# Kernel optimization log

Hardware: AMD Instinct MI355X
Metric: run time of the kernel (lower is better)

Reference implementation:

```python
import jax, jax.numpy as jnp
import numpy as np

D = 16        # d_model
DFF = 128     # ffn hidden
H_NN = 128    # pairwise-MLP hidden
RES = 1.0     # res_ratio (undefined global in source; standard residual)
EPS = 1e-6


def setup_inputs() -> dict:
    key = jax.random.key(0)
    ks = jax.random.split(key, 16)
    B, G, L = 8, 1, 256
    def n(k, shape, s=0.05):
        return jax.random.normal(k, shape, jnp.float32) * s
    return dict(
        x=jax.random.normal(ks[0], (B, G, L, D), jnp.float32),
        mask=jnp.zeros((B, G, L, L), jnp.float32),
        wq=n(ks[1], (D, D)), bq=jnp.zeros((D,), jnp.float32),
        wk=n(ks[2], (D, D)), bk=jnp.zeros((D,), jnp.float32),
        wv=n(ks[3], (D, D)), bv=jnp.zeros((D,), jnp.float32),
        wo=n(ks[4], (D, D)), bo=jnp.zeros((D,), jnp.float32),
        nn_w1=n(ks[5], (2 * D, H_NN)), nn_b1=jnp.zeros((H_NN,), jnp.float32),
        nn_w2=n(ks[6], (H_NN, 1)), nn_b2=jnp.zeros((1,), jnp.float32),
        f1=n(ks[7], (D, DFF)), f1b=jnp.zeros((DFF,), jnp.float32),
        f2=n(ks[8], (DFF, D)), f2b=jnp.zeros((D,), jnp.float32),
        g1=jnp.ones((D,), jnp.float32), be1=jnp.zeros((D,), jnp.float32),
        g2=jnp.ones((D,), jnp.float32), be2=jnp.zeros((D,), jnp.float32),
    )


def _layernorm(x, g, b):
    m = jnp.mean(x, -1, keepdims=True)
    v = jnp.var(x, -1, keepdims=True)
    return (x - m) * jax.lax.rsqrt(v + EPS) * g + b


def reference(x, mask, wq, bq, wk, bk, wv, bv, wo, bo,
              nn_w1, nn_b1, nn_w2, nn_b2,
              f1, f1b, f2, f2b, g1, be1, g2, be2):
    # projections: (B,G,L,D)
    q = x @ wq + bq
    k = x @ wk + bk
    v = x @ wv + bv
    # pairwise relation-network attention.
    # NN(concat([q_i, k_j])) first layer splits as q_i @ W1[:D] + k_j @ W1[D:]
    w1q, w1k = nn_w1[:D], nn_w1[D:]
    w2 = nn_w2[:, 0]
    qa = q @ w1q  # (B,G,L,H)
    kb = k @ w1k
    h1 = jax.nn.relu(qa[:, :, :, None, :] + kb[:, :, None, :, :] + nn_b1)  # (B,G,Lq,Lk,H)
    logits = jnp.einsum('bgijh,h->bgij', h1, w2) + nn_b2[0]
    # make_sym: NN(concat([k_j, q_i])) -> k_j @ W1[:D] + q_i @ W1[D:]
    ka = k @ w1q
    qb = q @ w1k
    h2 = jax.nn.relu(qb[:, :, :, None, :] + ka[:, :, None, :, :] + nn_b1)
    logits = logits + jnp.einsum('bgijh,h->bgij', h2, w2) + nn_b2[0]
    logits = logits + mask * -1e9
    attn = jax.nn.softmax(logits, axis=-1)          # (B,G,Lq,Lk)
    ctx = jnp.einsum('bgij,bgjd->bgid', attn, v)    # (B,G,L,D)
    attn_out = ctx @ wo + bo
    out1 = _layernorm(RES * x + (2.0 - RES) * attn_out, g1, be1)
    ffn = jax.nn.relu(out1 @ f1 + f1b) @ f2 + f2b
    out2 = _layernorm(RES * out1 + (2.0 - RES) * ffn, g2, be2)
    return out2
```

## Files before the change

kernel.cpp:

```cpp
#include <hip/hip_runtime.h>
#include <hip/hip_bf16.h>

typedef __hip_bfloat16 bf16;

constexpr int DIM  = 16;
constexpr int HNN  = 128;
constexpr int SEQ  = 256;
constexpr int BAT  = 8;
constexpr int ROWS = BAT * SEQ;

__device__ __forceinline__ bool is_f32(const void* g1) {
  return ((const unsigned*)g1)[0] == 0x3F800000u;
}
__device__ __forceinline__ float ld(const void* p, long i, bool f32) {
  return f32 ? ((const float*)p)[i]
             : __bfloat162float(((const bf16*)p)[i]);
}

__global__ __launch_bounds__(128) void prep_kernel(
    const void* __restrict__ x,
    const void* __restrict__ wq, const void* __restrict__ bq,
    const void* __restrict__ wk, const void* __restrict__ bk,
    const void* __restrict__ wv, const void* __restrict__ bv,
    const void* __restrict__ nn_w1, const void* __restrict__ nn_b1,
    const void* __restrict__ g1flag,
    float* __restrict__ qa, float* __restrict__ qb,
    float* __restrict__ kbT, float* __restrict__ kaT,
    float* __restrict__ vT)
{
  const bool f32 = is_f32(g1flag);
  const int row = blockIdx.x;
  const int tid = threadIdx.x;
  __shared__ float xs[DIM], qs[DIM], ks[DIM], vs[DIM];

  if (tid < DIM) xs[tid] = ld(x, (long)row * DIM + tid, f32);
  __syncthreads();

  if (tid < 3 * DIM) {
    const int which = tid >> 4, d = tid & 15;
    const void* w  = (which == 0) ? wq : (which == 1) ? wk : wv;
    const void* bb = (which == 0) ? bq : (which == 1) ? bk : bv;
    float acc = ld(bb, d, f32);
    #pragma unroll
    for (int e = 0; e < DIM; e++) acc += xs[e] * ld(w, e * DIM + d, f32);
    if (which == 0) qs[d] = acc;
    else if (which == 1) ks[d] = acc;
    else vs[d] = acc;
  }
  __syncthreads();

  float qw1q = 0.f, qw1k = 0.f, kw1q = 0.f, kw1k = 0.f;
  #pragma unroll
  for (int d = 0; d < DIM; d++) {
    float a = ld(nn_w1, d * HNN + tid, f32);
    float b = ld(nn_w1, (DIM + d) * HNN + tid, f32);
    qw1q += qs[d] * a;  qw1k += qs[d] * b;
    kw1q += ks[d] * a;  kw1k += ks[d] * b;
  }
  const float b1 = ld(nn_b1, tid, f32);
  qa[row * HNN + tid]   = qw1q;
  qb[row * HNN + tid]   = qw1k;
  kbT[tid * ROWS + row] = kw1k + b1;
  kaT[tid * ROWS + row] = kw1q + b1;
  if (tid < DIM) vT[tid * ROWS + row] = vs[tid];
}

__global__ __launch_bounds__(256) void attn_kernel(
    const void* __restrict__ x,  const void* __restrict__ mask,
    const void* __restrict__ wo, const void* __restrict__ bo,
    const void* __restrict__ nn_w2, const void* __restrict__ nn_b2,
    const void* __restrict__ f1, const void* __restrict__ f1b,
    const void* __restrict__ f2, const void* __restrict__ f2b,
    const void* __restrict__ g1, const void* __restrict__ be1,
    const void* __restrict__ g2, const void* __restrict__ be2,
    const float* __restrict__ qa, const float* __restrict__ qb,
    const float* __restrict__ kbT, const float* __restrict__ kaT,
    const float* __restrict__ vT,
    void* __restrict__ out)
{
  const bool f32 = is_f32(g1);
  const int blk = blockIdx.x;
  const int bi  = blk >> 8;
  const int j   = threadIdx.x;

  __shared__ float sqa[HNN], sqb[HNN], sw2[HNN];
  __shared__ float red[SEQ], pbuf[SEQ];
  __shared__ float part[DIM][17];
  __shared__ float ctxs[DIM], r1[DIM], o1[DIM], hid[HNN], r2[DIM];

  if (j < HNN) {
    sqa[j] = qa[(size_t)blk * HNN + j];
    sqb[j] = qb[(size_t)blk * HNN + j];
    sw2[j] = ld(nn_w2, j, f32);
  }
  __syncthreads();

  const int col = bi * SEQ + j;
  float acc = 0.f;
  #pragma unroll 4
  for (int h = 0; h < HNN; h++) {
    float kb = kbT[h * ROWS + col];
    float ka = kaT[h * ROWS + col];
    acc += sw2[h] * (fmaxf(sqa[h] + kb, 0.f) + fmaxf(sqb[h] + ka, 0.f));
  }
  float logit = acc + 2.f * ld(nn_b2, 0, f32)
              + ld(mask, (long)blk * SEQ + j, f32) * -1e9f;

  red[j] = logit;
  __syncthreads();
  for (int s = 128; s > 0; s >>= 1) {
    if (j < s) red[j] = fmaxf(red[j], red[j + s]);
    __syncthreads();
  }
  const float mx = red[0];
  __syncthreads();
  const float e = __expf(logit - mx);
  pbuf[j] = e;
  red[j]  = e;
  __syncthreads();
  for (int s = 128; s > 0; s >>= 1) {
    if (j < s) red[j] += red[j + s];
    __syncthreads();
  }
  const float inv = 1.f / red[0];

  {
    const int d = j & 15, c = j >> 4;
    float p = 0.f;
    #pragma unroll
    for (int jj = 0; jj < 16; jj++)
      p += pbuf[c * 16 + jj] * vT[d * ROWS + bi * SEQ + c * 16 + jj];
    part[d][c] = p;
  }
  __syncthreads();
  if (j < DIM) {
    float s = 0.f;
    #pragma unroll
    for (int c = 0; c < 16; c++) s += part[j][c];
    ctxs[j] = s * inv;
  }
  __syncthreads();

  if (j < DIM) {
    float ao = ld(bo, j, f32);
    #pragma unroll
    for (int d = 0; d < DIM; d++) ao += ctxs[d] * ld(wo, d * DIM + j, f32);
    r1[j] = ld(x, (long)blk * DIM + j, f32) + ao;
  }
  __syncthreads();

  if (j < DIM) {
    float m = 0.f;
    #pragma unroll
    for (int d = 0; d < DIM; d++) m += r1[d];
    m *= (1.f / DIM);
    float v = 0.f;
    #pragma unroll
    for (int d = 0; d < DIM; d++) { float t = r1[d] - m; v += t * t; }
    v *= (1.f / DIM);
    o1[j] = (r1[j] - m) * rsqrtf(v + 1e-6f) * ld(g1, j, f32) + ld(be1, j, f32);
  }
  __syncthreads();

  if (j < HNN) {
    float a = ld(f1b, j, f32);
    #pragma unroll
    for (int d = 0; d < DIM; d++) a += o1[d] * ld(f1, d * HNN + j, f32);
    hid[j] = fmaxf(a, 0.f);
  }
  __syncthreads();

  if (j < DIM) {
    float a = ld(f2b, j, f32);
    for (int h = 0; h < HNN; h++) a += hid[h] * ld(f2, h * DIM + j, f32);
    r2[j] = o1[j] + a;
  }
  __syncthreads();

  if (j < DIM) {
    float m = 0.f;
    #pragma unroll
    for (int d = 0; d < DIM; d++) m += r2[d];
    m *= (1.f / DIM);
    float v = 0.f;
    #pragma unroll
    for (int d = 0; d < DIM; d++) { float t = r2[d] - m; v += t * t; }
    v *= (1.f / DIM);
    float val = (r2[j] - m) * rsqrtf(v + 1e-6f) * ld(g2, j, f32) + ld(be2, j, f32);
    if (f32) ((float*)out)[(long)blk * DIM + j] = val;
    else     ((bf16*)out)[(long)blk * DIM + j] = __float2bfloat16(val);
  }
}

extern "C" void kernel_launch(void* const* d_in, const int* in_sizes, int n_in,
                              void* d_out, int out_size, void* d_ws, size_t ws_size,
                              hipStream_t stream) {
  const void* x     = d_in[0];
  const void* mask  = d_in[1];
  const void* wq    = d_in[2];
  const void* bq    = d_in[3];
  const void* wk    = d_in[4];
  const void* bk    = d_in[5];
  const void* wv    = d_in[6];
  const void* bv    = d_in[7];
  const void* wo    = d_in[8];
  const void* bo    = d_in[9];
  const void* nn_w1 = d_in[10];
  const void* nn_b1 = d_in[11];
  const void* nn_w2 = d_in[12];
  const void* nn_b2 = d_in[13];
  const void* f1    = d_in[14];
  const void* f1b   = d_in[15];
  const void* f2    = d_in[16];
  const void* f2b   = d_in[17];
  const void* g1    = d_in[18];
  const void* be1   = d_in[19];
  const void* g2    = d_in[20];
  const void* be2   = d_in[21];

  float* qa  = (float*)d_ws;
  float* qb  = qa  + (size_t)ROWS * HNN;
  float* kbT = qb  + (size_t)ROWS * HNN;
  float* kaT = kbT + (size_t)ROWS * HNN;
  float* vT  = kaT + (size_t)ROWS * HNN;

  prep_kernel<<<ROWS, 128, 0, stream>>>(x, wq, bq, wk, bk, wv, bv, nn_w1, nn_b1,
                                        g1, qa, qb, kbT, kaT, vT);
  attn_kernel<<<ROWS, 256, 0, stream>>>(x, mask, wo, bo, nn_w2, nn_b2,
                                        f1, f1b, f2, f2b, g1, be1, g2, be2,
                                        qa, qb, kbT, kaT, vT, d_out);
}
```

Measured before the change: 147.1 us.

## Process four query rows per block and interleave key tensors for float4 loads

The attention kernel now handles four query rows per block instead of one. Each loaded key feature (ka/kb, interleaved into a single float2-packed buffer so one float4 load fetches two hidden units) is reused across four queries, cutting global key traffic by roughly four. Block reductions are replaced by wavefront shuffles, V is staged in shared memory, and w2 is converted once in the prep kernel. The cost is more registers and shared memory per block and a quarter as many blocks, which lowers parallelism.

Result: faster. 138.0 us (-6.2%).

```diff
diff --git a/kernel.cpp b/kernel.cpp
--- a/kernel.cpp
+++ b/kernel.cpp
@@ -8,6 +8,8 @@
 constexpr int SEQ  = 256;
 constexpr int BAT  = 8;
 constexpr int ROWS = BAT * SEQ;
+constexpr int QT   = 4;
+constexpr int NBLK = ROWS / QT;
 
 __device__ __forceinline__ bool is_f32(const void* g1) {
   return ((const unsigned*)g1)[0] == 0x3F800000u;
@@ -23,10 +25,9 @@
     const void* __restrict__ wk, const void* __restrict__ bk,
     const void* __restrict__ wv, const void* __restrict__ bv,
     const void* __restrict__ nn_w1, const void* __restrict__ nn_b1,
-    const void* __restrict__ g1flag,
+    const void* __restrict__ nn_w2, const void* __restrict__ g1flag,
     float* __restrict__ qa, float* __restrict__ qb,
-    float* __restrict__ kbT, float* __restrict__ kaT,
-    float* __restrict__ vT)
+    float* __restrict__ kkT, float* __restrict__ vT, float* __restrict__ w2f)
 {
   const bool f32 = is_f32(g1flag);
   const int row = blockIdx.x;
@@ -58,137 +59,163 @@
     kw1q += ks[d] * a;  kw1k += ks[d] * b;
   }
   const float b1 = ld(nn_b1, tid, f32);
-  qa[row * HNN + tid]   = qw1q;
-  qb[row * HNN + tid]   = qw1k;
-  kbT[tid * ROWS + row] = kw1k + b1;
-  kaT[tid * ROWS + row] = kw1q + b1;
+  qa[row * HNN + tid] = qw1q;
+  qb[row * HNN + tid] = qw1k;
+  ((float2*)kkT)[((size_t)(tid >> 1) * ROWS + row) * 2 + (tid & 1)] =
+      make_float2(kw1k + b1, kw1q + b1);
   if (tid < DIM) vT[tid * ROWS + row] = vs[tid];
+  if (row == 0) w2f[tid] = ld(nn_w2, tid, f32);
 }
 
 __global__ __launch_bounds__(256) void attn_kernel(
     const void* __restrict__ x,  const void* __restrict__ mask,
     const void* __restrict__ wo, const void* __restrict__ bo,
-    const void* __restrict__ nn_w2, const void* __restrict__ nn_b2,
+    const void* __restrict__ nn_b2,
     const void* __restrict__ f1, const void* __restrict__ f1b,
     const void* __restrict__ f2, const void* __restrict__ f2b,
     const void* __restrict__ g1, const void* __restrict__ be1,
     const void* __restrict__ g2, const void* __restrict__ be2,
     const float* __restrict__ qa, const float* __restrict__ qb,
-    const float* __restrict__ kbT, const float* __restrict__ kaT,
-    const float* __restrict__ vT,
+    const float* __restrict__ kkT, const float* __restrict__ vT,
+    const float* __restrict__ w2f,
     void* __restrict__ out)
 {
   const bool f32 = is_f32(g1);
-  const int blk = blockIdx.x;
-  const int bi  = blk >> 8;
-  const int j   = threadIdx.x;
-
-  __shared__ float sqa[HNN], sqb[HNN], sw2[HNN];
-  __shared__ float red[SEQ], pbuf[SEQ];
-  __shared__ float part[DIM][17];
-  __shared__ float ctxs[DIM], r1[DIM], o1[DIM], hid[HNN], r2[DIM];
-
-  if (j < HNN) {
-    sqa[j] = qa[(size_t)blk * HNN + j];
-    sqb[j] = qb[(size_t)blk * HNN + j];
-    sw2[j] = ld(nn_w2, j, f32);
-  }
-  __syncthreads();
-
-  const int col = bi * SEQ + j;
-  float acc = 0.f;
-  #pragma unroll 4
-  for (int h = 0; h < HNN; h++) {
-    float kb = kbT[h * ROWS + col];
-    float ka = kaT[h * ROWS + col];
-    acc += sw2[h] * (fmaxf(sqa[h] + kb, 0.f) + fmaxf(sqb[h] + ka, 0.f));
-  }
-  float logit = acc + 2.f * ld(nn_b2, 0, f32)
-              + ld(mask, (long)blk * SEQ + j, f32) * -1e9f;
-
-  red[j] = logit;
-  __syncthreads();
-  for (int s = 128; s > 0; s >>= 1) {
-    if (j < s) red[j] = fmaxf(red[j], red[j + s]);
-    __syncthreads();
-  }
-  const float mx = red[0];
-  __syncthreads();
-  const float e = __expf(logit - mx);
-  pbuf[j] = e;
-  red[j]  = e;
-  __syncthreads();
-  for (int s = 128; s > 0; s >>= 1) {
-    if (j < s) red[j] += red[j + s];
-    __syncthreads();
-  }
-  const float inv = 1.f / red[0];
-
-  {
-    const int d = j & 15, c = j >> 4;
-    float p = 0.f;
-    #pragma unroll
-    for (int jj = 0; jj < 16; jj++)
-      p += pbuf[c * 16 + jj] * vT[d * ROWS + bi * SEQ + c * 16 + jj];
-    part[d][c] = p;
-  }
-  __syncthreads();
-  if (j < DIM) {
+  const int blk  = blockIdx.x;
+  const int bi   = blk >> 6;
+  const int i0   = (blk & 63) * QT;
+  const int t    = threadIdx.x;
+  const int j    = t;
+  const int col  = bi * SEQ + j;
+  const int lane = t & 63, wv = t >> 6;
+
+  __shared__ float pb[QT][SEQ];
+  __shared__ float vbufT[SEQ][DIM + 1];
+  __shared__ float wred[2][QT][4];
+  __shared__ float ctxs[QT][DIM];
+  __shared__ float tmpA[QT][DIM];
+  __shared__ float tmpB[QT][DIM];
+  __shared__ float hids[QT][HNN];
+
+  #pragma unroll
+  for (int d = 0; d < DIM; ++d) vbufT[j][d] = vT[d * ROWS + col];
+
+  const float* qaB = qa + (size_t)(bi * SEQ + i0) * HNN;
+  const float* qbB = qb + (size_t)(bi * SEQ + i0) * HNN;
+  float acc[QT] = {0.f, 0.f, 0.f, 0.f};
+  #pragma unroll 2
+  for (int hp = 0; hp < HNN / 2; ++hp) {
+    const float4 kk = ((const float4*)kkT)[(size_t)hp * ROWS + col];
+    const float w0 = w2f[2 * hp], w1 = w2f[2 * hp + 1];
+    #pragma unroll
+    for (int ii = 0; ii < QT; ++ii) {
+      const float* qai = qaB + ii * HNN;
+      const float* qbi = qbB + ii * HNN;
+      float s0 = fmaxf(qai[2 * hp]     + kk.x, 0.f) + fmaxf(qbi[2 * hp]     + kk.y, 0.f);
+      float s1 = fmaxf(qai[2 * hp + 1] + kk.z, 0.f) + fmaxf(qbi[2 * hp + 1] + kk.w, 0.f);
+      acc[ii] = fmaf(w0, s0, acc[ii]);
+      acc[ii] = fmaf(w1, s1, acc[ii]);
+    }
+  }
+
+  const float b2v = ld(nn_b2, 0, f32);
+  float la[QT], e[QT];
+  #pragma unroll
+  for (int ii = 0; ii < QT; ++ii)
+    la[ii] = acc[ii] + 2.f * b2v
+           + ld(mask, ((size_t)bi * SEQ + (i0 + ii)) * SEQ + j, f32) * -1e9f;
+
+  #pragma unroll
+  for (int ii = 0; ii < QT; ++ii) {
+    float m = la[ii];
+    #pragma unroll
+    for (int off = 32; off > 0; off >>= 1) m = fmaxf(m, __shfl_xor(m, off, 64));
+    if (lane == 0) wred[0][ii][wv] = m;
+  }
+  __syncthreads();
+  #pragma unroll
+  for (int ii = 0; ii < QT; ++ii) {
+    const float mx = fmaxf(fmaxf(wred[0][ii][0], wred[0][ii][1]),
+                           fmaxf(wred[0][ii][2], wred[0][ii][3]));
+    const float ev = __expf(la[ii] - mx);
+    e[ii] = ev;
+    float s = ev;
+    #pragma unroll
+    for (int off = 32; off > 0; off >>= 1) s += __shfl_xor(s, off, 64);
+    if (lane == 0) wred[1][ii][wv] = s;
+    pb[ii][j] = ev;
+  }
+  __syncthreads();
+
+  if (t < QT * DIM) {
+    const int ii = t >> 4, d = t & 15;
     float s = 0.f;
-    #pragma unroll
-    for (int c = 0; c < 16; c++) s += part[j][c];
-    ctxs[j] = s * inv;
-  }
-  __syncthreads();
-
-  if (j < DIM) {
-    float ao = ld(bo, j, f32);
-    #pragma unroll
-    for (int d = 0; d < DIM; d++) ao += ctxs[d] * ld(wo, d * DIM + j, f32);
-    r1[j] = ld(x, (long)blk * DIM + j, f32) + ao;
-  }
-  __syncthreads();
-
-  if (j < DIM) {
+    #pragma unroll 8
+    for (int jj = 0; jj < SEQ; ++jj) s += pb[ii][jj] * vbufT[jj][d];
+    const float inv = 1.f / (wred[1][ii][0] + wred[1][ii][1] +
+                             wred[1][ii][2] + wred[1][ii][3]);
+    ctxs[ii][d] = s * inv;
+  }
+  __syncthreads();
+
+  if (t < QT * DIM) {
+    const int ii = t >> 4, d = t & 15;
+    float ao = ld(bo, d, f32);
+    #pragma unroll
+    for (int dd = 0; dd < DIM; ++dd) ao += ctxs[ii][dd] * ld(wo, dd * DIM + d, f32);
+    tmpA[ii][d] = ld(x, ((size_t)(bi * SEQ + i0 + ii)) * DIM + d, f32) + ao;
+  }
+  __syncthreads();
+
+  if (t < QT * DIM) {
+    const int ii = t >> 4, d = t & 15;
     float m = 0.f;
     #pragma unroll
-    for (int d = 0; d < DIM; d++) m += r1[d];
+    for (int dd = 0; dd < DIM; ++dd) m += tmpA[ii][dd];
     m *= (1.f / DIM);
     float v = 0.f;
     #pragma unroll
-    for (int d = 0; d < DIM; d++) { float t = r1[d] - m; v += t * t; }
+    for (int dd = 0; dd < DIM; ++dd) { float z = tmpA[ii][dd] - m; v += z * z; }
     v *= (1.f / DIM);
-    o1[j] = (r1[j] - m) * rsqrtf(v + 1e-6f) * ld(g1, j, f32) + ld(be1, j, f32);
-  }
-  __syncthreads();
-
-  if (j < HNN) {
-    float a = ld(f1b, j, f32);
-    #pragma unroll
-    for (int d = 0; d < DIM; d++) a += o1[d] * ld(f1, d * HNN + j, f32);
-    hid[j] = fmaxf(a, 0.f);
-  }
-  __syncthreads();
-
-  if (j < DIM) {
-    float a = ld(f2b, j, f32);
-    for (int h = 0; h < HNN; h++) a += hid[h] * ld(f2, h * DIM + j, f32);
-    r2[j] = o1[j] + a;
-  }
-  __syncthreads();
-
-  if (j < DIM) {
+    tmpB[ii][d] = (tmpA[ii][d] - m) * rsqrtf(v + 1e-6f) * ld(g1, d, f32)
+                + ld(be1, d, f32);
+  }
+  __syncthreads();
+
+  #pragma unroll
+  for (int p = 0; p < 2; ++p) {
+    const int ii = (t >> 7) + 2 * p;
+    const int h  = t & 127;
+    float a = ld(f1b, h, f32);
+    #pragma unroll
+    for (int dd = 0; dd < DIM; ++dd) a += tmpB[ii][dd] * ld(f1, dd * HNN + h, f32);
+    hids[ii][h] = fmaxf(a, 0.f);
+  }
+  __syncthreads();
+
+  if (t < QT * DIM) {
+    const int ii = t >> 4, d = t & 15;
+    float a = ld(f2b, d, f32);
+    for (int h = 0; h < HNN; ++h) a += hids[ii][h] * ld(f2, h * DIM + d, f32);
+    tmpA[ii][d] = tmpB[ii][d] + a;
+  }
+  __syncthreads();
+
+  if (t < QT * DIM) {
+    const int ii = t >> 4, d = t & 15;
     float m = 0.f;
     #pragma unroll
-    for (int d = 0; d < DIM; d++) m += r2[d];
+    for (int dd = 0; dd < DIM; ++dd) m += tmpA[ii][dd];
     m *= (1.f / DIM);
     float v = 0.f;
     #pragma unroll
-    for (int d = 0; d < DIM; d++) { float t = r2[d] - m; v += t * t; }
+    for (int dd = 0; dd < DIM; ++dd) { float z = tmpA[ii][dd] - m; v += z * z; }
     v *= (1.f / DIM);
-    float val = (r2[j] - m) * rsqrtf(v + 1e-6f) * ld(g2, j, f32) + ld(be2, j, f32);
-    if (f32) ((float*)out)[(long)blk * DIM + j] = val;
-    else     ((bf16*)out)[(long)blk * DIM + j] = __float2bfloat16(val);
+    const float val = (tmpA[ii][d] - m) * rsqrtf(v + 1e-6f) * ld(g2, d, f32)
+                    + ld(be2, d, f32);
+    const long oidx = ((long)(bi * SEQ + i0 + ii)) * DIM + d;
+    if (f32) ((float*)out)[oidx] = val;
+    else     ((bf16*)out)[oidx] = __float2bfloat16(val);
   }
 }
 
@@ -220,13 +247,13 @@
 
   float* qa  = (float*)d_ws;
   float* qb  = qa  + (size_t)ROWS * HNN;
-  float* kbT = qb  + (size_t)ROWS * HNN;
-  float* kaT = kbT + (size_t)ROWS * HNN;
-  float* vT  = kaT + (size_t)ROWS * HNN;
+  float* kkT = qb  + (size_t)ROWS * HNN;
+  float* vT  = kkT + (size_t)ROWS * HNN * 2;
+  float* w2f = vT  + (size_t)DIM * ROWS;
 
   prep_kernel<<<ROWS, 128, 0, stream>>>(x, wq, bq, wk, bk, wv, bv, nn_w1, nn_b1,
-                                        g1, qa, qb, kbT, kaT, vT);
-  attn_kernel<<<ROWS, 256, 0, stream>>>(x, mask, wo, bo, nn_w2, nn_b2,
+                                        nn_w2, g1, qa, qb, kkT, vT, w2f);
+  attn_kernel<<<NBLK, 256, 0, stream>>>(x, mask, wo, bo, nn_b2,
                                         f1, f1b, f2, f2b, g1, be1, g2, be2,
-                                        qa, qb, kbT, kaT, vT, d_out);
-}
+                                        qa, qb, kkT, vT, w2f, d_out);
+}
```

## Split pairwise logits into query-tiled kernel with split-H partials and shuffle softmax

Applied to the files above, without the earlier changes.

Moves the pairwise relation-MLP logit computation into its own kernel. Each block handles 4 queries and one quarter of the hidden dimension, so every loaded key feature is reused across 4 queries, and float4-interleaved ka/kb layouts vectorize the loads. Partial logits are written to a workspace and summed in a tail kernel. The tail kernel uses wave shuffles for the softmax reductions, stages V in shared memory and parallelizes the FFN second layer. This adds a third launch and an extra global round-trip of 4×ROWS×SEQ partial logits in exchange for less redundant key traffic and more parallelism.

Result: faster. 127.1 us (-13.6%).

```diff
diff --git a/kernel.cpp b/kernel.cpp
--- a/kernel.cpp
+++ b/kernel.cpp
@@ -8,6 +8,10 @@
 constexpr int SEQ  = 256;
 constexpr int BAT  = 8;
 constexpr int ROWS = BAT * SEQ;
+constexpr int HP   = HNN / 2;
+constexpr int QT   = 4;
+constexpr int NQT  = ROWS / QT;
+constexpr int QHP  = 16;
 
 __device__ __forceinline__ bool is_f32(const void* g1) {
   return ((const unsigned*)g1)[0] == 0x3F800000u;
@@ -23,10 +27,9 @@
     const void* __restrict__ wk, const void* __restrict__ bk,
     const void* __restrict__ wv, const void* __restrict__ bv,
     const void* __restrict__ nn_w1, const void* __restrict__ nn_b1,
-    const void* __restrict__ g1flag,
-    float* __restrict__ qa, float* __restrict__ qb,
-    float* __restrict__ kbT, float* __restrict__ kaT,
-    float* __restrict__ vT)
+    const void* __restrict__ nn_w2, const void* __restrict__ g1flag,
+    float* __restrict__ kkT, float* __restrict__ qq,
+    float* __restrict__ vT,  float2* __restrict__ w2p)
 {
   const bool f32 = is_f32(g1flag);
   const int row = blockIdx.x;
@@ -58,137 +61,187 @@
     kw1q += ks[d] * a;  kw1k += ks[d] * b;
   }
   const float b1 = ld(nn_b1, tid, f32);
-  qa[row * HNN + tid]   = qw1q;
-  qb[row * HNN + tid]   = qw1k;
-  kbT[tid * ROWS + row] = kw1k + b1;
-  kaT[tid * ROWS + row] = kw1q + b1;
+  const int hp = tid >> 1, half = tid & 1;
+  ((float2*)kkT)[((size_t)hp * ROWS + row) * 2 + half] =
+      make_float2(kw1k + b1, kw1q + b1);
+  ((float2*)qq)[((size_t)row * HP + hp) * 2 + half] =
+      make_float2(qw1q, qw1k);
   if (tid < DIM) vT[tid * ROWS + row] = vs[tid];
-}
-
-__global__ __launch_bounds__(256) void attn_kernel(
+  if (row == 0 && tid < HP)
+    w2p[tid] = make_float2(ld(nn_w2, 2 * tid, f32), ld(nn_w2, 2 * tid + 1, f32));
+}
+
+__global__ __launch_bounds__(256) void logits_kernel(
+    const float4* __restrict__ kkT, const float4* __restrict__ qq,
+    const float2* __restrict__ w2p, float* __restrict__ part)
+{
+  const int bid     = blockIdx.x;
+  const int qt      = bid & (NQT - 1);
+  const int quarter = bid >> 9;
+  const int bi = qt >> 6;
+  const int i0 = (qt & 63) * QT;
+  const int j  = threadIdx.x;
+  const int col = bi * SEQ + j;
+
+  __shared__ float4 sqq[QT][QHP];
+  __shared__ float2 sw2[QHP];
+
+  if (j < QT * QHP) {
+    const int ii = j >> 4, m = j & 15;
+    sqq[ii][m] = qq[(size_t)(bi * SEQ + i0 + ii) * HP + quarter * QHP + m];
+  }
+  if (j < QHP) sw2[j] = w2p[quarter * QHP + j];
+  __syncthreads();
+
+  float acc0 = 0.f, acc1 = 0.f, acc2 = 0.f, acc3 = 0.f;
+  const float4* kkbase = kkT + (size_t)quarter * QHP * ROWS + col;
+  #pragma unroll 8
+  for (int m = 0; m < QHP; ++m) {
+    const float4 kk = kkbase[(size_t)m * ROWS];
+    const float2 w  = sw2[m];
+    const float4 q0 = sqq[0][m], q1 = sqq[1][m], q2 = sqq[2][m], q3 = sqq[3][m];
+    acc0 += w.x * (fmaxf(q0.x + kk.x, 0.f) + fmaxf(q0.y + kk.y, 0.f))
+          + w.y * (fmaxf(q0.z + kk.z, 0.f) + fmaxf(q0.w + kk.w, 0.f));
+    acc1 += w.x * (fmaxf(q1.x + kk.x, 0.f) + fmaxf(q1.y + kk.y, 0.f))
+          + w.y * (fmaxf(q1.z + kk.z, 0.f) + fmaxf(q1.w + kk.w, 0.f));
+    acc2 += w.x * (fmaxf(q2.x + kk.x, 0.f) + fmaxf(q2.y + kk.y, 0.f))
+          + w.y * (fmaxf(q2.z + kk.z, 0.f) + fmaxf(q2.w + kk.w, 0.f));
+    acc3 += w.x * (fmaxf(q3.x + kk.x, 0.f) + fmaxf(q3.y + kk.y, 0.f))
+          + w.y * (fmaxf(q3.z + kk.z, 0.f) + fmaxf(q3.w + kk.w, 0.f));
+  }
+  float* dst = part + ((size_t)quarter * ROWS + (bi * SEQ + i0)) * SEQ + j;
+  dst[0 * SEQ] = acc0;
+  dst[1 * SEQ] = acc1;
+  dst[2 * SEQ] = acc2;
+  dst[3 * SEQ] = acc3;
+}
+
+__global__ __launch_bounds__(256) void tail_kernel(
     const void* __restrict__ x,  const void* __restrict__ mask,
     const void* __restrict__ wo, const void* __restrict__ bo,
-    const void* __restrict__ nn_w2, const void* __restrict__ nn_b2,
+    const void* __restrict__ nn_b2,
     const void* __restrict__ f1, const void* __restrict__ f1b,
     const void* __restrict__ f2, const void* __restrict__ f2b,
     const void* __restrict__ g1, const void* __restrict__ be1,
     const void* __restrict__ g2, const void* __restrict__ be2,
-    const float* __restrict__ qa, const float* __restrict__ qb,
-    const float* __restrict__ kbT, const float* __restrict__ kaT,
-    const float* __restrict__ vT,
+    const float* __restrict__ part, const float* __restrict__ vT,
     void* __restrict__ out)
 {
   const bool f32 = is_f32(g1);
-  const int blk = blockIdx.x;
-  const int bi  = blk >> 8;
-  const int j   = threadIdx.x;
-
-  __shared__ float sqa[HNN], sqb[HNN], sw2[HNN];
-  __shared__ float red[SEQ], pbuf[SEQ];
-  __shared__ float part[DIM][17];
-  __shared__ float ctxs[DIM], r1[DIM], o1[DIM], hid[HNN], r2[DIM];
-
-  if (j < HNN) {
-    sqa[j] = qa[(size_t)blk * HNN + j];
-    sqb[j] = qb[(size_t)blk * HNN + j];
-    sw2[j] = ld(nn_w2, j, f32);
-  }
-  __syncthreads();
-
-  const int col = bi * SEQ + j;
-  float acc = 0.f;
-  #pragma unroll 4
-  for (int h = 0; h < HNN; h++) {
-    float kb = kbT[h * ROWS + col];
-    float ka = kaT[h * ROWS + col];
-    acc += sw2[h] * (fmaxf(sqa[h] + kb, 0.f) + fmaxf(sqb[h] + ka, 0.f));
-  }
-  float logit = acc + 2.f * ld(nn_b2, 0, f32)
-              + ld(mask, (long)blk * SEQ + j, f32) * -1e9f;
-
-  red[j] = logit;
-  __syncthreads();
-  for (int s = 128; s > 0; s >>= 1) {
-    if (j < s) red[j] = fmaxf(red[j], red[j + s]);
-    __syncthreads();
-  }
-  const float mx = red[0];
-  __syncthreads();
+  const int qidx = blockIdx.x;
+  const int bi   = qidx >> 8;
+  const int j    = threadIdx.x;
+  const int col  = bi * SEQ + j;
+  const int lane = j & 63, wvi = j >> 6;
+
+  __shared__ float pb[SEQ];
+  __shared__ float vbuf[SEQ][DIM + 1];
+  __shared__ float red[2][4];
+  __shared__ float cpart[DIM][17];
+  __shared__ float ctxs[DIM], rr[DIM], o1[DIM], hid[HNN];
+
+  #pragma unroll
+  for (int d = 0; d < DIM; ++d) vbuf[j][d] = vT[d * ROWS + col];
+
+  const float* pp = part + (size_t)qidx * SEQ + j;
+  const size_t QS = (size_t)ROWS * SEQ;
+  float logit = pp[0] + pp[QS] + pp[2 * QS] + pp[3 * QS]
+              + 2.f * ld(nn_b2, 0, f32)
+              + ld(mask, (size_t)qidx * SEQ + j, f32) * -1e9f;
+
+  float m = logit;
+  #pragma unroll
+  for (int off = 32; off > 0; off >>= 1) m = fmaxf(m, __shfl_xor(m, off, 64));
+  if (lane == 0) red[0][wvi] = m;
+  __syncthreads();
+  const float mx = fmaxf(fmaxf(red[0][0], red[0][1]), fmaxf(red[0][2], red[0][3]));
   const float e = __expf(logit - mx);
-  pbuf[j] = e;
-  red[j]  = e;
-  __syncthreads();
-  for (int s = 128; s > 0; s >>= 1) {
-    if (j < s) red[j] += red[j + s];
-    __syncthreads();
-  }
-  const float inv = 1.f / red[0];
+  pb[j] = e;
+  float s = e;
+  #pragma unroll
+  for (int off = 32; off > 0; off >>= 1) s += __shfl_xor(s, off, 64);
+  if (lane == 0) red[1][wvi] = s;
+  __syncthreads();
+  const float inv = 1.f / (red[1][0] + red[1][1] + red[1][2] + red[1][3]);
 
   {
     const int d = j & 15, c = j >> 4;
-    float p = 0.f;
-    #pragma unroll
-    for (int jj = 0; jj < 16; jj++)
-      p += pbuf[c * 16 + jj] * vT[d * ROWS + bi * SEQ + c * 16 + jj];
-    part[d][c] = p;
-  }
-  __syncthreads();
-  if (j < DIM) {
-    float s = 0.f;
-    #pragma unroll
-    for (int c = 0; c < 16; c++) s += part[j][c];
-    ctxs[j] = s * inv;
+    float sacc = 0.f;
+    #pragma unroll
+    for (int jj = 0; jj < 16; ++jj)
+      sacc += pb[c * 16 + jj] * vbuf[c * 16 + jj][d];
+    cpart[d][c] = sacc;
+  }
+  __syncthreads();
+  if (j < DIM) {
+    float sc = 0.f;
+    #pragma unroll
+    for (int c = 0; c < 16; ++c) sc += cpart[j][c];
+    ctxs[j] = sc * inv;
   }
   __syncthreads();
 
   if (j < DIM) {
     float ao = ld(bo, j, f32);
     #pragma unroll
-    for (int d = 0; d < DIM; d++) ao += ctxs[d] * ld(wo, d * DIM + j, f32);
-    r1[j] = ld(x, (long)blk * DIM + j, f32) + ao;
-  }
-  __syncthreads();
-
-  if (j < DIM) {
-    float m = 0.f;
-    #pragma unroll
-    for (int d = 0; d < DIM; d++) m += r1[d];
-    m *= (1.f / DIM);
-    float v = 0.f;
-    #pragma unroll
-    for (int d = 0; d < DIM; d++) { float t = r1[d] - m; v += t * t; }
-    v *= (1.f / DIM);
-    o1[j] = (r1[j] - m) * rsqrtf(v + 1e-6f) * ld(g1, j, f32) + ld(be1, j, f32);
+    for (int dd = 0; dd < DIM; ++dd) ao += ctxs[dd] * ld(wo, dd * DIM + j, f32);
+    rr[j] = ld(x, (long)qidx * DIM + j, f32) + ao;
+  }
+  __syncthreads();
+  if (j < DIM) {
+    float mn = 0.f;
+    #pragma unroll
+    for (int dd = 0; dd < DIM; ++dd) mn += rr[dd];
+    mn *= (1.f / DIM);
+    float vv = 0.f;
+    #pragma unroll
+    for (int dd = 0; dd < DIM; ++dd) { float z = rr[dd] - mn; vv += z * z; }
+    vv *= (1.f / DIM);
+    o1[j] = (rr[j] - mn) * rsqrtf(vv + 1e-6f) * ld(g1, j, f32) + ld(be1, j, f32);
   }
   __syncthreads();
 
   if (j < HNN) {
     float a = ld(f1b, j, f32);
     #pragma unroll
-    for (int d = 0; d < DIM; d++) a += o1[d] * ld(f1, d * HNN + j, f32);
+    for (int dd = 0; dd < DIM; ++dd) a += o1[dd] * ld(f1, dd * HNN + j, f32);
     hid[j] = fmaxf(a, 0.f);
   }
   __syncthreads();
 
+  {
+    const int d = j & 15, c = j >> 4;
+    float a = 0.f;
+    #pragma unroll
+    for (int hh = 0; hh < 8; ++hh) {
+      const int h = c * 8 + hh;
+      a += hid[h] * ld(f2, h * DIM + d, f32);
+    }
+    cpart[d][c] = a;
+  }
+  __syncthreads();
   if (j < DIM) {
     float a = ld(f2b, j, f32);
-    for (int h = 0; h < HNN; h++) a += hid[h] * ld(f2, h * DIM + j, f32);
-    r2[j] = o1[j] + a;
-  }
-  __syncthreads();
-
-  if (j < DIM) {
-    float m = 0.f;
-    #pragma unroll
-    for (int d = 0; d < DIM; d++) m += r2[d];
-    m *= (1.f / DIM);
-    float v = 0.f;
-    #pragma unroll
-    for (int d = 0; d < DIM; d++) { float t = r2[d] - m; v += t * t; }
-    v *= (1.f / DIM);
-    float val = (r2[j] - m) * rsqrtf(v + 1e-6f) * ld(g2, j, f32) + ld(be2, j, f32);
-    if (f32) ((float*)out)[(long)blk * DIM + j] = val;
-    else     ((bf16*)out)[(long)blk * DIM + j] = __float2bfloat16(val);
+    #pragma unroll
+    for (int c = 0; c < 16; ++c) a += cpart[j][c];
+    rr[j] = o1[j] + a;
+  }
+  __syncthreads();
+
+  if (j < DIM) {
+    float mn = 0.f;
+    #pragma unroll
+    for (int dd = 0; dd < DIM; ++dd) mn += rr[dd];
+    mn *= (1.f / DIM);
+    float vv = 0.f;
+    #pragma unroll
+    for (int dd = 0; dd < DIM; ++dd) { float z = rr[dd] - mn; vv += z * z; }
+    vv *= (1.f / DIM);
+    const float val = (rr[j] - mn) * rsqrtf(vv + 1e-6f) * ld(g2, j, f32)
+                    + ld(be2, j, f32);
+    const long oidx = (long)qidx * DIM + j;
+    if (f32) ((float*)out)[oidx] = val;
+    else     ((bf16*)out)[oidx] = __float2bfloat16(val);
   }
 }
 
@@ -218,15 +271,18 @@
   const void* g2    = d_in[20];
   const void* be2   = d_in[21];
 
-  float* qa  = (float*)d_ws;
-  float* qb  = qa  + (size_t)ROWS * HNN;
-  float* kbT = qb  + (size_t)ROWS * HNN;
-  float* kaT = kbT + (size_t)ROWS * HNN;
-  float* vT  = kaT + (size_t)ROWS * HNN;
-
-  prep_kernel<<<ROWS, 128, 0, stream>>>(x, wq, bq, wk, bk, wv, bv, nn_w1, nn_b1,
-                                        g1, qa, qb, kbT, kaT, vT);
-  attn_kernel<<<ROWS, 256, 0, stream>>>(x, mask, wo, bo, nn_w2, nn_b2,
+  float*  kkT  = (float*)d_ws;
+  float*  qq   = kkT + (size_t)HP * ROWS * 4;
+  float*  vT   = qq  + (size_t)ROWS * HP * 4;
+  float*  part = vT  + (size_t)DIM * ROWS;
+  float2* w2p  = (float2*)(part + (size_t)4 * ROWS * SEQ);
+
+  prep_kernel<<<ROWS, 128, 0, stream>>>(x, wq, bq, wk, bk, wv, bv,
+                                        nn_w1, nn_b1, nn_w2, g1,
+                                        kkT, qq, vT, w2p);
+  logits_kernel<<<4 * NQT, 256, 0, stream>>>((const float4*)kkT, (const float4*)qq,
+                                             (const float2*)w2p, part);
+  tail_kernel<<<ROWS, 256, 0, stream>>>(x, mask, wo, bo, nn_b2,
                                         f1, f1b, f2, f2b, g1, be1, g2, be2,
-                                        qa, qb, kbT, kaT, vT, d_out);
-}
+                                        part, vT, d_out);
+}
```
